# Kernel tuning notes

Measured on AMD Instinct MI355X. Metric: run time of the kernel, lower is better.

Reference implementation:

```python
import jax, jax.numpy as jnp
import numpy as np

N_NODES = 100000
N_EDGES = 1600000
NEG_SLOPE = 0.2


def gat_layer(x, edge_index, W, att_src, att_dst, bias, concat):
    """PyG-style GATConv (v1) with self-loops added, dropout=0."""
    N = x.shape[0]
    H, C = att_src.shape
    ar = jnp.arange(N)
    src = jnp.concatenate([edge_index[0], ar])  # add self-loops
    dst = jnp.concatenate([edge_index[1], ar])
    h = (x @ W).reshape(N, H, C)                # [N,H,C]
    a_src = jnp.sum(h * att_src[None], axis=-1)  # [N,H]
    a_dst = jnp.sum(h * att_dst[None], axis=-1)  # [N,H]
    e = jax.nn.leaky_relu(a_src[src] + a_dst[dst], NEG_SLOPE)  # [E,H]
    # segment softmax over destination nodes
    m = jax.ops.segment_max(e, dst, num_segments=N)
    e = jnp.exp(e - m[dst])
    s = jax.ops.segment_sum(e, dst, num_segments=N)
    alpha = e / (s[dst] + 1e-16)                # [E,H]
    msg = h[src] * alpha[:, :, None]            # [E,H,C]
    out = jax.ops.segment_sum(msg, dst, num_segments=N)  # [N,H,C]
    if concat:
        out = out.reshape(N, H * C)
    else:
        out = out.mean(axis=1)
    return out + bias


def prelu(x, a):
    return jnp.where(x >= 0, x, a * x)


def setup_inputs() -> dict:
    key = jax.random.key(0)
    ks = jax.random.split(key, 12)
    def g(k, shape, fan):
        return jax.random.normal(k, shape, dtype=jnp.float32) * (1.0 / np.sqrt(fan))
    x = jax.random.normal(ks[0], (N_NODES, 256), dtype=jnp.float32)
    edge_index = jax.random.randint(ks[1], (2, N_EDGES), 0, N_NODES, dtype=jnp.int64 if jax.config.read('jax_enable_x64') else jnp.int32)
    return {
        'x': x,
        'edge_index': edge_index,
        'W1': g(ks[2], (256, 64), 256), 'as1': g(ks[3], (8, 8), 8), 'ad1': g(ks[4], (8, 8), 8), 'b1': jnp.zeros((64,), jnp.float32),
        'W2': g(ks[5], (320, 64), 320), 'as2': g(ks[6], (8, 8), 8), 'ad2': g(ks[7], (8, 8), 8), 'b2': jnp.zeros((64,), jnp.float32),
        'W3': g(ks[8], (64, 128), 64), 'as3': g(ks[9], (8, 16), 16), 'ad3': g(ks[10], (8, 16), 16), 'b3': jnp.zeros((16,), jnp.float32),
        'p1': jnp.full((1,), 0.25, jnp.float32), 'p2': jnp.full((1,), 0.25, jnp.float32),
    }


def reference(x, edge_index, W1, as1, ad1, b1, W2, as2, ad2, b2, W3, as3, ad3, b3, p1, p2):
    h = gat_layer(x, edge_index, W1, as1, ad1, b1, concat=True)
    h = prelu(h, p1)
    h = gat_layer(jnp.concatenate([x, h], axis=1), edge_index, W2, as2, ad2, b2, concat=True)
    h = prelu(h, p2)
    h = gat_layer(h, edge_index, W3, as3, ad3, b3, concat=False)
    return jax.nn.log_softmax(h, axis=1)
```

## Files before the change

### kernel.cpp

```cpp
#include <hip/hip_runtime.h>
#include <hip/hip_bf16.h>
#include <stdint.h>

typedef unsigned short u16;
typedef __attribute__((ext_vector_type(8))) short short8;
typedef __attribute__((ext_vector_type(8))) __bf16 bf16x8;
typedef __attribute__((ext_vector_type(4))) float f32x4;
typedef __attribute__((ext_vector_type(4))) float fv4;

#define DEV static __device__ __forceinline__

DEV float bf2f(u16 u) { uint32_t i = ((uint32_t)u) << 16; float f; __builtin_memcpy(&f, &i, 4); return f; }
DEV u16 f2bf(float f) {
    uint32_t i; __builtin_memcpy(&i, &f, 4);
    uint32_t r = i + 0x7FFFu + ((i >> 16) & 1u);
    return (u16)(r >> 16);
}
DEV float lo16f(uint32_t u) { uint32_t i = u << 16; float f; __builtin_memcpy(&f, &i, 4); return f; }
DEV float hi16f(uint32_t u) { uint32_t i = u & 0xFFFF0000u; float f; __builtin_memcpy(&f, &i, 4); return f; }
DEV uint32_t pack2(float a, float b) { return (uint32_t)f2bf(a) | ((uint32_t)f2bf(b) << 16); }
DEV float lrelu(float x) { return x >= 0.f ? x : 0.2f * x; }

#define CHK 4096
#define BN2SH 10
#define BN2 1024

__global__ __launch_bounds__(256) void k_cvt(const float* __restrict__ in, u16* __restrict__ out, int n4) {
    int i = blockIdx.x * 256 + threadIdx.x;
    if (i < n4) {
        fv4 v = __builtin_nontemporal_load((const fv4*)in + i);
        uint64_t o = (uint64_t)f2bf(v.x) | ((uint64_t)f2bf(v.y) << 16)
                   | ((uint64_t)f2bf(v.z) << 32) | ((uint64_t)f2bf(v.w) << 48);
        __builtin_nontemporal_store(o, (uint64_t*)out + i);
    }
}

__global__ __launch_bounds__(256) void k_hist(const int* __restrict__ dst, int* __restrict__ hist,
                                              int NBUK, int nbp, int E) {
    __shared__ int h[BN2];
    int tid = threadIdx.x;
    for (int i = tid; i < NBUK; i += 256) h[i] = 0;
    __syncthreads();
    int b0 = blockIdx.x * CHK;
    int jend = b0 + CHK < E ? b0 + CHK : E;
    for (int j = b0 + tid; j < jend; j += 256)
        atomicAdd(&h[dst[j] >> BN2SH], 1);
    __syncthreads();
    for (int i = tid; i < NBUK; i += 256) hist[i * nbp + blockIdx.x] = h[i];
}

__global__ void k_scanpart(const int* __restrict__ deg, int* __restrict__ bsum, int n) {
    __shared__ int buf[1024];
    int tid = threadIdx.x;
    int i = blockIdx.x * 1024 + tid;
    int v = (i < n) ? deg[i] : 0;
    buf[tid] = v; __syncthreads();
    for (int d = 512; d > 0; d >>= 1) {
        if (tid < d) buf[tid] += buf[tid + d];
        __syncthreads();
    }
    if (tid == 0) bsum[blockIdx.x] = buf[0];
}

__global__ void k_scanbsum(int* bsum, int nb) {
    if (threadIdx.x == 0) {
        int run = 0;
        for (int b = 0; b < nb; ++b) { int t = bsum[b]; bsum[b] = run; run += t; }
    }
}

__global__ void k_scanonly(const int* __restrict__ in, const int* __restrict__ bsum,
                           int* __restrict__ out, int n) {
    __shared__ int buf[1024];
    int tid = threadIdx.x;
    int i = blockIdx.x * 1024 + tid;
    int v = (i < n) ? in[i] : 0;
    buf[tid] = v; __syncthreads();
    for (int d = 1; d < 1024; d <<= 1) {
        int t = (tid >= d) ? buf[tid - d] : 0;
        __syncthreads();
        buf[tid] += t;
        __syncthreads();
    }
    if (i < n) out[i] = buf[tid] - v + bsum[blockIdx.x];
}

__global__ __launch_bounds__(256) void k_part(const int* __restrict__ src, const int* __restrict__ dst,
                                              const int* __restrict__ scanned, int* __restrict__ stage,
                                              int NBUK, int nbp, int E) {
    __shared__ int cur[BN2];
    int tid = threadIdx.x;
    for (int i = tid; i < NBUK; i += 256) cur[i] = scanned[i * nbp + blockIdx.x];
    __syncthreads();
    int b0 = blockIdx.x * CHK;
    int jend = b0 + CHK < E ? b0 + CHK : E;
    for (int j = b0 + tid; j < jend; j += 256) {
        int d = dst[j];
        int p = atomicAdd(&cur[d >> BN2SH], 1);
        stage[p] = src[j] | ((d & (BN2 - 1)) << 17);
    }
}

__global__ __launch_bounds__(256) void k_csr(const int* __restrict__ stage, const int* __restrict__ scanned,
                                             int* __restrict__ off, int* __restrict__ srt,
                                             int NBUK, int nbp, int N, int E) {
    __shared__ int deg[BN2];
    __shared__ int ex[BN2];
    __shared__ int tsum[256];
    int tid = threadIdx.x, b = blockIdx.x;
    int base = b << BN2SH;
    int s0 = scanned[b * nbp];
    int s1 = (b + 1 < NBUK) ? scanned[(b + 1) * nbp] : E;
    for (int i = tid; i < BN2; i += 256) deg[i] = 0;
    __syncthreads();
    for (int j = s0 + tid; j < s1; j += 256) atomicAdd(&deg[(uint32_t)stage[j] >> 17], 1);
    __syncthreads();
    int t4 = tid * 4;
    int d0 = deg[t4], d1 = deg[t4 + 1], d2 = deg[t4 + 2], d3 = deg[t4 + 3];
    int tot = d0 + d1 + d2 + d3;
    tsum[tid] = tot; __syncthreads();
    for (int d = 1; d < 256; d <<= 1) {
        int t = (tid >= d) ? tsum[tid - d] : 0;
        __syncthreads();
        tsum[tid] += t;
        __syncthreads();
    }
    int ebase = tsum[tid] - tot;
    ex[t4] = ebase; ex[t4 + 1] = ebase + d0; ex[t4 + 2] = ebase + d0 + d1; ex[t4 + 3] = ebase + d0 + d1 + d2;
    __syncthreads();
    for (int i = tid; i < BN2; i += 256) { int n = base + i; if (n < N) off[n] = s0 + ex[i]; }
    if (b == 0 && tid == 0) off[N] = E;
    __syncthreads();
    for (int j = s0 + tid; j < s1; j += 256) {
        int sd = stage[j];
        int p = atomicAdd(&ex[(uint32_t)sd >> 17], 1);
        srt[s0 + p] = sd & 0x1FFFF;
    }
}

__global__ __launch_bounds__(256) void gemm_k(const u16* __restrict__ A1, int K1,
                                              const u16* __restrict__ A2, int K2,
                                              const float* __restrict__ W, int M,
                                              u16* __restrict__ out, int N,
                                              const float* __restrict__ ats, const float* __restrict__ atd,
                                              float* __restrict__ a_src, float* __restrict__ a_dst, int hs) {
    __shared__ u16 wt[64][328];
    __shared__ u16 As[64][40];
    const int K = K1 + K2;
    const int tid = threadIdx.x;
    const int n0 = blockIdx.x * 64;
    const int cb = blockIdx.y * 64;

    for (int idx = tid; idx < K * 64; idx += 256) {
        int k = idx >> 6, m = idx & 63;
        wt[m][k] = f2bf(W[(size_t)k * M + cb + m]);
    }

    const int wv = tid >> 6, lane = tid & 63;
    const int quad = lane >> 4, r = lane & 15;
    f32x4 acc[4];
#pragma unroll
    for (int ct = 0; ct < 4; ++ct) acc[ct] = (f32x4){0.f, 0.f, 0.f, 0.f};

    const int row = tid >> 2, seg = tid & 3;
    const int gl = n0 + row;

    for (int k0 = 0; k0 < K; k0 += 32) {
        int4 v = {0, 0, 0, 0};
        if (gl < N) {
            const u16* base = (k0 < K1) ? (A1 + (size_t)gl * K1 + k0)
                                        : (A2 + (size_t)gl * K2 + (k0 - K1));
            v = *(const int4*)(base + seg * 8);
        }
        *(int4*)&As[row][seg * 8] = v;
        __syncthreads();
        bf16x8 a = __builtin_bit_cast(bf16x8, *(const short8*)&As[wv * 16 + r][quad * 8]);
#pragma unroll
        for (int ct = 0; ct < 4; ++ct) {
            bf16x8 b = __builtin_bit_cast(bf16x8, *(const short8*)&wt[ct * 16 + r][k0 + quad * 8]);
            acc[ct] = __builtin_amdgcn_mfma_f32_16x16x32_bf16(a, b, acc[ct], 0, 0, 0);
        }
        __syncthreads();
    }

    const int rmask = (1 << hs) - 1;
#pragma unroll
    for (int ct = 0; ct < 4; ++ct)
#pragma unroll
        for (int rg = 0; rg < 4; ++rg) {
            int grow = n0 + wv * 16 + quad * 4 + rg;
            float p = acc[ct][rg];
            if (grow < N) out[(size_t)grow * M + cb + ct * 16 + r] = f2bf(p);
            int col = cb + ct * 16 + r;
            float ps = p * ats[col];
            float pd = p * atd[col];
            ps += __shfl_xor(ps, 1); pd += __shfl_xor(pd, 1);
            ps += __shfl_xor(ps, 2); pd += __shfl_xor(pd, 2);
            ps += __shfl_xor(ps, 4); pd += __shfl_xor(pd, 4);
            if (rmask == 15) { ps += __shfl_xor(ps, 8); pd += __shfl_xor(pd, 8); }
            if ((r & rmask) == 0 && grow < N) {
                int head = col >> hs;
                a_src[grow * 8 + head] = ps;
                a_dst[grow * 8 + head] = pd;
            }
        }
}

__global__ __launch_bounds__(256) void agg12(const u16* __restrict__ g,
                                             const float* __restrict__ a_src, const float* __restrict__ a_dst,
                                             const int* __restrict__ off, const int* __restrict__ srt,
                                             const float* __restrict__ bias, const float* __restrict__ pslope,
                                             u16* __restrict__ hout, int N) {
    int tid = threadIdx.x;
    int lane32 = tid & 31;
    int node = blockIdx.x * 8 + (tid >> 5);
    int nd = node < N ? node : N - 1;
    int lane16 = lane32 & 15;
    int sub    = lane32 >> 4;
    int hg     = lane16 >> 1;
    int hw     = lane32 & 7;
    int e4     = lane32 >> 3;
    const char* gb = (const char*)g;

    float ad_acc = a_dst[nd * 8 + hg];
    float ad_w   = a_dst[nd * 8 + hw];
    float ws = __expf(lrelu(a_src[nd * 8 + hg] + ad_acc));
    float m0 = (sub == 0) ? ws : 0.f;
    uint2 gs = *(const uint2*)(gb + ((size_t)nd << 7) + lane16 * 8);
    float s = m0;
    float acc0 = m0 * lo16f(gs.x), acc1 = m0 * hi16f(gs.x);
    float acc2 = m0 * lo16f(gs.y), acc3 = m0 * hi16f(gs.y);

    int jb = off[nd], je = off[nd + 1];
    int addrH = (tid & 32) * 4;
    int addrS = addrH + sub * 32;
    int addrW = addrS + hg * 4;
    int laneoff = lane16 * 8;

    int idx = 0; float asv = 0.f;
    if (jb < je) {
        int jc = jb + e4; jc = jc < je ? jc : je - 1;
        idx = srt[jc];
        asv = a_src[idx * 8 + hw];
    }
    for (int j = jb; j < je; j += 4) {
        float w = __expf(lrelu(asv + ad_w));
        w = (j + e4 < je) ? w : 0.f;
        int wi = __builtin_bit_cast(int, w);
        int jn = j + 4 + e4; jn = jn < je ? jn : je - 1;
        int idx_n = srt[jn];
        float as_n = a_src[idx_n * 8 + hw];

        int sv0 = __builtin_amdgcn_ds_bpermute(addrS,      idx);
        int wb0 = __builtin_amdgcn_ds_bpermute(addrW,      wi);
        int sv1 = __builtin_amdgcn_ds_bpermute(addrS + 64, idx);
        int wb1 = __builtin_amdgcn_ds_bpermute(addrW + 64, wi);
        uint2 g0 = *(const uint2*)(gb + (((uint32_t)sv0 << 7) + laneoff));
        uint2 g1 = *(const uint2*)(gb + (((uint32_t)sv1 << 7) + laneoff));
        float wv0 = __builtin_bit_cast(float, wb0);
        float wv1 = __builtin_bit_cast(float, wb1);
        s += wv0;
        acc0 += wv0 * lo16f(g0.x); acc1 += wv0 * hi16f(g0.x);
        acc2 += wv0 * lo16f(g0.y); acc3 += wv0 * hi16f(g0.y);
        s += wv1;
        acc0 += wv1 * lo16f(g1.x); acc1 += wv1 * hi16f(g1.x);
        acc2 += wv1 * lo16f(g1.y); acc3 += wv1 * hi16f(g1.y);
        idx = idx_n; asv = as_n;
    }
    s    += __shfl_xor(s,    16);
    acc0 += __shfl_xor(acc0, 16); acc1 += __shfl_xor(acc1, 16);
    acc2 += __shfl_xor(acc2, 16); acc3 += __shfl_xor(acc3, 16);
    if (node < N && sub == 0) {
        float r = 1.f / (s + 1e-16f);
        fv4 bv = *(const fv4*)(bias + lane16 * 4);
        float p = pslope[0];
        float v0 = acc0 * r + bv.x; v0 = v0 >= 0.f ? v0 : p * v0;
        float v1 = acc1 * r + bv.y; v1 = v1 >= 0.f ? v1 : p * v1;
        float v2 = acc2 * r + bv.z; v2 = v2 >= 0.f ? v2 : p * v2;
        float v3 = acc3 * r + bv.w; v3 = v3 >= 0.f ? v3 : p * v3;
        uint2 o; o.x = pack2(v0, v1); o.y = pack2(v2, v3);
        *(uint2*)((char*)hout + ((size_t)node << 7) + lane16 * 8) = o;
    }
}

__global__ __launch_bounds__(256) void agg3(const u16* __restrict__ g,
                                            const float* __restrict__ a_src, const float* __restrict__ a_dst,
                                            const int* __restrict__ off, const int* __restrict__ srt,
                                            const float* __restrict__ b3, float* __restrict__ out, int N) {
    int tid = threadIdx.x;
    int lane = tid & 63;
    int node = blockIdx.x * 4 + (tid >> 6);
    int nd = node < N ? node : N - 1;
    int lane32 = lane & 31;
    int sub = lane >> 5;
    int hg = lane32 >> 2;
    int hw = lane & 7;
    int e8 = lane >> 3;
    const char* gb = (const char*)g;

    float ad_acc = a_dst[nd * 8 + hg];
    float ad_w   = a_dst[nd * 8 + hw];
    float ws = __expf(lrelu(a_src[nd * 8 + hg] + ad_acc));
    float m0 = (sub == 0) ? ws : 0.f;
    uint2 gs = *(const uint2*)(gb + ((size_t)nd << 8) + lane32 * 8);
    float s = m0;
    float acc0 = m0 * lo16f(gs.x), acc1 = m0 * hi16f(gs.x);
    float acc2 = m0 * lo16f(gs.y), acc3 = m0 * hi16f(gs.y);

    int jb = off[nd], je = off[nd + 1];
    int addrS = sub * 32;
    int addrW = addrS + hg * 4;
    int laneoff = lane32 * 8;

    int idx = 0; float asv = 0.f;
    if (jb < je) {
        int jc = jb + e8; jc = jc < je ? jc : je - 1;
        idx = srt[jc];
        asv = a_src[idx * 8 + hw];
    }
    for (int j = jb; j < je; j += 8) {
        float w = __expf(lrelu(asv + ad_w));
        w = (j + e8 < je) ? w : 0.f;
        int wi = __builtin_bit_cast(int, w);
        int jn = j + 8 + e8; jn = jn < je ? jn : je - 1;
        int idx_n = srt[jn];
        float as_n = a_src[idx_n * 8 + hw];
#pragma unroll
        for (int t = 0; t < 4; ++t) {
            int sv = __builtin_amdgcn_ds_bpermute(addrS + t * 64, idx);
            int wb = __builtin_amdgcn_ds_bpermute(addrW + t * 64, wi);
            uint2 gv = *(const uint2*)(gb + (((uint32_t)sv << 8) + laneoff));
            float wf = __builtin_bit_cast(float, wb);
            s += wf;
            acc0 += wf * lo16f(gv.x); acc1 += wf * hi16f(gv.x);
            acc2 += wf * lo16f(gv.y); acc3 += wf * hi16f(gv.y);
        }
        idx = idx_n; asv = as_n;
    }
    s    += __shfl_xor(s,    32);
    acc0 += __shfl_xor(acc0, 32); acc1 += __shfl_xor(acc1, 32);
    acc2 += __shfl_xor(acc2, 32); acc3 += __shfl_xor(acc3, 32);
    float r = 1.f / (s + 1e-16f);
    acc0 *= r; acc1 *= r; acc2 *= r; acc3 *= r;
#pragma unroll
    for (int d = 4; d <= 16; d <<= 1) {
        acc0 += __shfl_xor(acc0, d); acc1 += __shfl_xor(acc1, d);
        acc2 += __shfl_xor(acc2, d); acc3 += __shfl_xor(acc3, d);
    }
    fv4 bv = *(const fv4*)(b3 + (lane32 & 3) * 4);
    float v0 = acc0 * 0.125f + bv.x;
    float v1 = acc1 * 0.125f + bv.y;
    float v2 = acc2 * 0.125f + bv.z;
    float v3 = acc3 * 0.125f + bv.w;
    float m = fmaxf(fmaxf(v0, v1), fmaxf(v2, v3));
    m = fmaxf(m, __shfl_xor(m, 1)); m = fmaxf(m, __shfl_xor(m, 2));
    float se = __expf(v0 - m) + __expf(v1 - m) + __expf(v2 - m) + __expf(v3 - m);
    se += __shfl_xor(se, 1); se += __shfl_xor(se, 2);
    float lg = __logf(se);
    if (node < N && lane < 4) {
        float4 o;
        o.x = v0 - m - lg; o.y = v1 - m - lg; o.z = v2 - m - lg; o.w = v3 - m - lg;
        *(float4*)(out + (size_t)node * 16 + lane * 4) = o;
    }
}

extern "C" void kernel_launch(void* const* d_in, const int* in_sizes, int n_in,
                              void* d_out, int out_size, void* d_ws, size_t ws_size,
                              hipStream_t stream) {
    (void)n_in; (void)out_size; (void)ws_size;
    const float* x  = (const float*)d_in[0];
    const int* ei   = (const int*)d_in[1];
    const float* W1 = (const float*)d_in[2];
    const float* as1 = (const float*)d_in[3];
    const float* ad1 = (const float*)d_in[4];
    const float* b1  = (const float*)d_in[5];
    const float* W2  = (const float*)d_in[6];
    const float* as2 = (const float*)d_in[7];
    const float* ad2 = (const float*)d_in[8];
    const float* b2  = (const float*)d_in[9];
    const float* W3  = (const float*)d_in[10];
    const float* as3 = (const float*)d_in[11];
    const float* ad3 = (const float*)d_in[12];
    const float* b3  = (const float*)d_in[13];
    const float* p1  = (const float*)d_in[14];
    const float* p2  = (const float*)d_in[15];
    const int N = in_sizes[0] / 256;
    const int E = in_sizes[1] / 2;
    const int NBUK = (N + BN2 - 1) >> BN2SH;
    const int nbp = (E + CHK - 1) / CHK;
    const int nsc = NBUK * nbp;

    char* ws = (char*)d_ws;
    size_t o = 0;
    auto alloc = [&](size_t bytes) { void* p = ws + o; o = (o + bytes + 255) & ~(size_t)255; return p; };
    int* off     = (int*)alloc((size_t)(N + 1) * 4);
    int* bsum    = (int*)alloc(4096);
    int* hist    = (int*)alloc((size_t)nsc * 4);
    int* scanned = (int*)alloc((size_t)nsc * 4);
    int* srt     = (int*)alloc((size_t)E * 4);
    int* stage   = (int*)alloc((size_t)E * 4);
    u16* xb      = (u16*)alloc((size_t)N * 256 * 2);
    u16* g       = (u16*)alloc((size_t)N * 128 * 2);
    float* a_src = (float*)alloc((size_t)N * 8 * 4);
    float* a_dst = (float*)alloc((size_t)N * 8 * 4);
    u16* h1      = (u16*)alloc((size_t)N * 64 * 2);
    u16* h2      = (u16*)alloc((size_t)N * 64 * 2);

    int n4 = N * 256 / 4;
    k_cvt<<<(n4 + 255) / 256, 256, 0, stream>>>(x, xb, n4);

    k_hist<<<nbp, 256, 0, stream>>>(ei + E, hist, NBUK, nbp, E);
    int nS = (nsc + 1023) / 1024;
    k_scanpart<<<nS, 1024, 0, stream>>>(hist, bsum, nsc);
    k_scanbsum<<<1, 64, 0, stream>>>(bsum, nS);
    k_scanonly<<<nS, 1024, 0, stream>>>(hist, bsum, scanned, nsc);
    k_part<<<nbp, 256, 0, stream>>>(ei, ei + E, scanned, stage, NBUK, nbp, E);
    k_csr<<<NBUK, 256, 0, stream>>>(stage, scanned, off, srt, NBUK, nbp, N, E);

    int nb64 = (N + 63) / 64;
    int nb4 = (N + 3) / 4;
    int nb8 = (N + 7) / 8;

    gemm_k<<<dim3(nb64, 1), 256, 0, stream>>>(xb, 256, (const u16*)nullptr, 0, W1, 64, g, N,
                                              as1, ad1, a_src, a_dst, 3);
    agg12<<<nb8, 256, 0, stream>>>(g, a_src, a_dst, off, srt, b1, p1, h1, N);

    gemm_k<<<dim3(nb64, 1), 256, 0, stream>>>(xb, 256, h1, 64, W2, 64, g, N,
                                              as2, ad2, a_src, a_dst, 3);
    agg12<<<nb8, 256, 0, stream>>>(g, a_src, a_dst, off, srt, b2, p2, h2, N);

    gemm_k<<<dim3(nb64, 2), 256, 0, stream>>>(h2, 64, (const u16*)nullptr, 0, W3, 128, g, N,
                                              as3, ad3, a_src, a_dst, 4);
    agg3<<<nb4, 256, 0, stream>>>(g, a_src, a_dst, off, srt, b3, (float*)d_out, N);
}
```

Before: 577.0 us.

## Restructure GEMM weight staging into k-chunked LDS layout and load A directly

Repacks the bf16 weight tile in shared memory into 8-element k-chunks so that each MFMA B operand is one contiguous 16-byte read. The A-tile staging through shared memory is removed: each lane loads its A row fragment straight from global memory, which drops the two barriers per k-step. The attention coefficients are hoisted out of the inner epilogue loop. Without LDS staging, A loads are now per-lane 16-byte global reads that are not coalesced across a row and nothing is prefetched.

```diff
diff --git a/kernel.cpp b/kernel.cpp
--- a/kernel.cpp
+++ b/kernel.cpp
@@ -144,17 +144,28 @@
                                               u16* __restrict__ out, int N,
                                               const float* __restrict__ ats, const float* __restrict__ atd,
                                               float* __restrict__ a_src, float* __restrict__ a_dst, int hs) {
-    __shared__ u16 wt[64][328];
-    __shared__ u16 As[64][40];
+    __shared__ u16 wt2[40][64][8];
     const int K = K1 + K2;
+    const int nc = K >> 3;
     const int tid = threadIdx.x;
     const int n0 = blockIdx.x * 64;
     const int cb = blockIdx.y * 64;
 
-    for (int idx = tid; idx < K * 64; idx += 256) {
-        int k = idx >> 6, m = idx & 63;
-        wt[m][k] = f2bf(W[(size_t)k * M + cb + m]);
-    }
+    for (int p = tid; p < (nc << 6); p += 256) {
+        int c = p >> 6, m = p & 63;
+        const float* wp = W + ((size_t)(c << 3)) * M + cb + m;
+        uint64_t w0 = (uint64_t)f2bf(wp[0])
+                    | ((uint64_t)f2bf(wp[(size_t)M]) << 16)
+                    | ((uint64_t)f2bf(wp[(size_t)2 * M]) << 32)
+                    | ((uint64_t)f2bf(wp[(size_t)3 * M]) << 48);
+        uint64_t w1 = (uint64_t)f2bf(wp[(size_t)4 * M])
+                    | ((uint64_t)f2bf(wp[(size_t)5 * M]) << 16)
+                    | ((uint64_t)f2bf(wp[(size_t)6 * M]) << 32)
+                    | ((uint64_t)f2bf(wp[(size_t)7 * M]) << 48);
+        uint64_t* d = (uint64_t*)&wt2[c][m][0];
+        d[0] = w0; d[1] = w1;
+    }
+    __syncthreads();
 
     const int wv = tid >> 6, lane = tid & 63;
     const int quad = lane >> 4, r = lane & 15;
@@ -162,38 +173,37 @@
 #pragma unroll
     for (int ct = 0; ct < 4; ++ct) acc[ct] = (f32x4){0.f, 0.f, 0.f, 0.f};
 
-    const int row = tid >> 2, seg = tid & 3;
-    const int gl = n0 + row;
-
-    for (int k0 = 0; k0 < K; k0 += 32) {
-        int4 v = {0, 0, 0, 0};
-        if (gl < N) {
-            const u16* base = (k0 < K1) ? (A1 + (size_t)gl * K1 + k0)
-                                        : (A2 + (size_t)gl * K2 + (k0 - K1));
-            v = *(const int4*)(base + seg * 8);
-        }
-        *(int4*)&As[row][seg * 8] = v;
-        __syncthreads();
-        bf16x8 a = __builtin_bit_cast(bf16x8, *(const short8*)&As[wv * 16 + r][quad * 8]);
+    int arow = n0 + wv * 16 + r;
+    int ar = arow < N ? arow : N - 1;
+    const u16* rowA1 = A1 + (size_t)ar * K1;
+    const u16* rowA2 = A2 ? (A2 + (size_t)ar * K2 - K1) : rowA1;
+
+    const int nit = K >> 5;
+    for (int it = 0; it < nit; ++it) {
+        int kk = (it << 5) + quad * 8;
+        const u16* ap = (kk < K1) ? (rowA1 + kk) : (rowA2 + kk);
+        bf16x8 a = __builtin_bit_cast(bf16x8, *(const short8*)ap);
+        int cbase = it << 2;
 #pragma unroll
         for (int ct = 0; ct < 4; ++ct) {
-            bf16x8 b = __builtin_bit_cast(bf16x8, *(const short8*)&wt[ct * 16 + r][k0 + quad * 8]);
+            bf16x8 b = __builtin_bit_cast(bf16x8, *(const short8*)&wt2[cbase + quad][ct * 16 + r][0]);
             acc[ct] = __builtin_amdgcn_mfma_f32_16x16x32_bf16(a, b, acc[ct], 0, 0, 0);
         }
-        __syncthreads();
     }
 
     const int rmask = (1 << hs) - 1;
 #pragma unroll
-    for (int ct = 0; ct < 4; ++ct)
+    for (int ct = 0; ct < 4; ++ct) {
+        int col = cb + ct * 16 + r;
+        float as_c = ats[col];
+        float ad_c = atd[col];
 #pragma unroll
         for (int rg = 0; rg < 4; ++rg) {
             int grow = n0 + wv * 16 + quad * 4 + rg;
             float p = acc[ct][rg];
-            if (grow < N) out[(size_t)grow * M + cb + ct * 16 + r] = f2bf(p);
-            int col = cb + ct * 16 + r;
-            float ps = p * ats[col];
-            float pd = p * atd[col];
+            if (grow < N) out[(size_t)grow * M + col] = f2bf(p);
+            float ps = p * as_c;
+            float pd = p * ad_c;
             ps += __shfl_xor(ps, 1); pd += __shfl_xor(pd, 1);
             ps += __shfl_xor(ps, 2); pd += __shfl_xor(pd, 2);
             ps += __shfl_xor(ps, 4); pd += __shfl_xor(pd, 4);
@@ -204,6 +214,7 @@
                 a_dst[grow * 8 + head] = pd;
             }
         }
+    }
 }
 
 __global__ __launch_bounds__(256) void agg12(const u16* __restrict__ g,
```

Measured after the change: 534.3 us. 7.4% less time.
